# Kernel tuning notes

Measured on AMD Instinct MI355X. Metric: run time of the kernel, lower is better.

The kernel has to match this reference:

```python
import jax, jax.numpy as jnp
import numpy as np

MODEL_DIM = 4096
HEAD_DIM = 128
N_HEADS = 32
N_KV_HEADS = 8
B = 2
S = 2048
ROPE_BASE = 10000.0


def _rope(v, pos):
    """Interleaved-pair rotary embedding (Llama style). v: [b, s, h, d]."""
    d = v.shape[-1]
    half = d // 2
    inv_freq = 1.0 / (ROPE_BASE ** (jnp.arange(half, dtype=jnp.float32) * 2.0 / d))
    t = pos + jnp.arange(v.shape[1], dtype=jnp.float32)          # [s]
    ang = t[:, None] * inv_freq                                   # [s, half]
    cos = jnp.cos(ang)[None, :, None, :].astype(v.dtype)          # [1, s, 1, half]
    sin = jnp.sin(ang)[None, :, None, :].astype(v.dtype)
    x1 = v[..., 0::2]
    x2 = v[..., 1::2]
    o1 = x1 * cos - x2 * sin
    o2 = x1 * sin + x2 * cos
    return jnp.stack([o1, o2], axis=-1).reshape(v.shape)


def setup_inputs() -> dict:
    key = jax.random.key(0)
    kx, kq, kk, kv, ko = jax.random.split(key, 5)
    wscale = MODEL_DIM ** -0.5  # keep pre-softmax logits in a sane range
    x = jax.random.normal(kx, (B, S, MODEL_DIM), dtype=jnp.float32)
    wq = jax.random.normal(kq, (HEAD_DIM * N_HEADS, MODEL_DIM), dtype=jnp.float32) * wscale
    wk = jax.random.normal(kk, (HEAD_DIM * N_KV_HEADS, MODEL_DIM), dtype=jnp.float32) * wscale
    wv = jax.random.normal(kv, (HEAD_DIM * N_KV_HEADS, MODEL_DIM), dtype=jnp.float32) * wscale
    wo = jax.random.normal(ko, (HEAD_DIM * N_HEADS, MODEL_DIM), dtype=jnp.float32).T * wscale
    wo = jnp.asarray(wo)  # [MODEL_DIM, HEAD_DIM*N_HEADS] like nn.Linear weight
    # causal additive mask, as SDPA attn_mask (float): 0 on/below diag, -inf above
    causal = jnp.tril(jnp.ones((S, S), dtype=bool))
    mask = jnp.where(causal, 0.0, -jnp.inf).astype(jnp.float32)
    return {"x": x, "wq": wq, "wk": wk, "wv": wv, "wo": wo, "mask": mask, "pos": 0}


def reference(x, wq, wk, wv, wo, mask, pos):
    b, s, _ = x.shape
    rep = N_HEADS // N_KV_HEADS
    q = (x @ wq.T).reshape(b, s, N_HEADS, HEAD_DIM)
    k = (x @ wk.T).reshape(b, s, N_KV_HEADS, HEAD_DIM)
    v = (x @ wv.T).reshape(b, s, N_KV_HEADS, HEAD_DIM)
    q = _rope(q, pos)
    k = _rope(k, pos)
    # With pos=0 prefill, the kv-cache slice [:, :pos+s] equals k, v just written.
    # GQA without materializing repeat_interleave: group q heads by kv head.
    qg = q.reshape(b, s, N_KV_HEADS, rep, HEAD_DIM)
    scale = HEAD_DIM ** -0.5
    scores = jnp.einsum('bqhrd,bkhd->bhrqk', qg, k) * scale        # [b, kvh, rep, s, s]
    scores = scores + mask                                          # broadcast [s, s]
    p = jax.nn.softmax(scores, axis=-1)
    out = jnp.einsum('bhrqk,bkhd->bqhrd', p, v).reshape(b, s, N_HEADS * HEAD_DIM)
    return out @ wo.T
```

## Files before the change

kernel.cpp:

```cpp
#include <hip/hip_runtime.h>
#include <hip/hip_bf16.h>
#include <stdint.h>

#define MODEL_DIM 4096
#define HEAD_DIM  128
#define NH        32
#define NKV       8
#define BB        2
#define SS        2048
#define ROWS      (BB*SS)
#define QKVN      (MODEL_DIM + 2*NKV*HEAD_DIM)
#define KOFF      MODEL_DIM
#define VOFF      (MODEL_DIM + NKV*HEAD_DIM)
#define SCALE_QK  0.08838834764831845f

typedef __attribute__((ext_vector_type(8))) short short8;
typedef __attribute__((ext_vector_type(4))) float f32x4;

static __device__ __forceinline__ unsigned short f2bf(float f) {
  union { float f; unsigned u; } v; v.f = f;
  unsigned r = v.u + 0x7fffu + ((v.u >> 16) & 1u);
  return (unsigned short)(r >> 16);
}
static __device__ __forceinline__ float bf2f(unsigned short u) {
  union { unsigned u; float f; } v; v.u = ((unsigned)u) << 16;
  return v.f;
}
static __device__ __forceinline__ void glds16(const unsigned short* g, const unsigned short* l) {
  __builtin_amdgcn_global_load_lds((const __attribute__((address_space(1))) void*)g,
      (__attribute__((address_space(3))) void*)l, 16, 0, 0);
}

__global__ void cvt_bf16(const float* __restrict__ s, unsigned short* __restrict__ d, int n4) {
  int i = blockIdx.x * blockDim.x + threadIdx.x;
  int st = gridDim.x * blockDim.x;
  for (; i < n4; i += st) {
    float4 v = reinterpret_cast<const float4*>(s)[i];
    ushort4 o;
    o.x = f2bf(v.x); o.y = f2bf(v.y); o.z = f2bf(v.z); o.w = f2bf(v.w);
    reinterpret_cast<ushort4*>(d)[i] = o;
  }
}

template<int OUT_F32>
__global__ __launch_bounds__(256) void gemm_bt(
    const unsigned short* __restrict__ A, const unsigned short* __restrict__ B,
    void* __restrict__ Cv, int M, int N, int K)
{
  __shared__ unsigned short As[128 * 32];
  __shared__ unsigned short Bs[128 * 32];
  const int tid  = threadIdx.x;
  const int lane = tid & 63;
  const int w    = tid >> 6;

  const int nwg = gridDim.x;
  const int bid = blockIdx.x;
  const int q8  = nwg >> 3;
  const int wg  = (bid & 7) * q8 + (bid >> 3);
  const int gm  = M >> 7;
  const int bm  = wg % gm, bn = wg / gm;
  const int m0  = bm << 7, n0 = bn << 7;
  const int wm  = (w >> 1) << 6, wn = (w & 1) << 6;

  f32x4 acc[4][4] = {};

  const int rowA = lane >> 2;
  const int ch8  = (lane & 3) * 8;

  for (int k0 = 0; k0 < K; k0 += 32) {
    __syncthreads();
    #pragma unroll
    for (int i = 0; i < 2; ++i) {
      const unsigned short* ga = A + (size_t)(m0 + i*64 + w*16 + rowA) * K + k0 + ch8;
      glds16(ga, &As[(i*64 + w*16) * 32]);
      const unsigned short* gb = B + (size_t)(n0 + i*64 + w*16 + rowA) * K + k0 + ch8;
      glds16(gb, &Bs[(i*64 + w*16) * 32]);
    }
    __syncthreads();

    short8 af[4], bf[4];
    const int fr = lane & 15, fg = lane >> 4;
    #pragma unroll
    for (int r = 0; r < 4; ++r)
      af[r] = *(const short8*)&As[(wm + r*16 + fr) * 32 + fg * 8];
    #pragma unroll
    for (int r = 0; r < 4; ++r)
      bf[r] = *(const short8*)&Bs[(wn + r*16 + fr) * 32 + fg * 8];
    #pragma unroll
    for (int i = 0; i < 4; ++i)
      #pragma unroll
      for (int j = 0; j < 4; ++j)
        acc[i][j] = __builtin_amdgcn_mfma_f32_16x16x32_bf16(af[i], bf[j], acc[i][j], 0, 0, 0);
  }

  const int cr = (lane >> 4) * 4, cc = lane & 15;
  #pragma unroll
  for (int i = 0; i < 4; ++i)
    #pragma unroll
    for (int j = 0; j < 4; ++j) {
      const int gr = m0 + wm + i*16 + cr;
      const int gc = n0 + wn + j*16 + cc;
      #pragma unroll
      for (int e = 0; e < 4; ++e) {
        const float v = acc[i][j][e];
        if (OUT_F32) ((float*)Cv)[(size_t)(gr + e) * N + gc] = v;
        else ((unsigned short*)Cv)[(size_t)(gr + e) * N + gc] = f2bf(v);
      }
    }
}

__global__ void rope_kernel(unsigned short* __restrict__ qkv, const int* __restrict__ posp) {
  const int row = blockIdx.x;
  const float t = (float)((row & (SS - 1)) + posp[0]);
  const float c0 = -13.28771237954945f / 64.0f;
  for (int i = threadIdx.x; i < (NH + NKV) * 64; i += blockDim.x) {
    const int hh = i >> 6, p = i & 63;
    const int colbase = (hh < NH) ? hh * HEAD_DIM : KOFF + (hh - NH) * HEAD_DIM;
    const float inv = exp2f((float)p * c0);
    float sn, cs;
    sincosf(t * inv, &sn, &cs);
    const size_t base = (size_t)row * QKVN + colbase + 2 * p;
    const float x1 = bf2f(qkv[base]), x2 = bf2f(qkv[base + 1]);
    qkv[base]     = f2bf(x1 * cs - x2 * sn);
    qkv[base + 1] = f2bf(x1 * sn + x2 * cs);
  }
}

__global__ __launch_bounds__(256) void vtrans_kernel(
    const unsigned short* __restrict__ qkv, unsigned short* __restrict__ vt)
{
  __shared__ unsigned short T[64 * 128];
  const int tid = threadIdx.x;
  const int bk  = blockIdx.y;
  const int s0  = blockIdx.x * 64;
  const int b   = bk >> 3, kvh = bk & 7;

  #pragma unroll
  for (int it = 0; it < 4; ++it) {
    const int cid  = it * 256 + tid;
    const int s    = cid >> 4, slot = cid & 15;
    const int sl   = (slot & 8) | ((slot ^ (s >> 3)) & 7);
    *(uint4*)&T[s * 128 + sl * 8] =
      *(const uint4*)&qkv[(size_t)(b * SS + s0 + s) * QKVN + VOFF + kvh * HEAD_DIM + slot * 8];
  }
  __syncthreads();
  #pragma unroll
  for (int it = 0; it < 4; ++it) {
    const int cid = it * 256 + tid;
    const int d   = cid >> 3, s8 = (cid & 7) * 8;
    unsigned short tmp[8];
    #pragma unroll
    for (int j = 0; j < 8; ++j) {
      const int s    = s8 + j;
      const int slot = d >> 3;
      const int sl   = (slot & 8) | ((slot ^ (s >> 3)) & 7);
      tmp[j] = T[s * 128 + sl * 8 + (d & 7)];
    }
    *(uint4*)&vt[((size_t)bk * HEAD_DIM + d) * SS + s0 + s8] = *(uint4*)tmp;
  }
}

#define QBLK 64
#define KVB  64
#define LDP  72

static __device__ __forceinline__ float bcast_row16(float v0, float v1, float v2, float v3, int lane) {
  const int sel = (lane >> 2) & 3;
  const float a = (sel & 1) ? v1 : v0;
  const float b = (sel & 1) ? v3 : v2;
  const float m = (sel & 2) ? b : a;
  const int q = lane & 15;
  return __shfl(m, ((q >> 2) << 4) + ((q & 3) << 2));
}

__global__ __launch_bounds__(256) void attn_kernel(
    const unsigned short* __restrict__ qkv, const unsigned short* __restrict__ vt,
    unsigned short* __restrict__ out)
{
  __shared__ unsigned short Kb[2][KVB * HEAD_DIM];
  __shared__ unsigned short Vb[2][HEAD_DIM * KVB];
  __shared__ unsigned short Ps[4 * 16 * LDP];

  const int tid  = threadIdx.x;
  const int lane = tid & 63;
  const int w    = tid >> 6;
  const int bh   = blockIdx.y;
  const int b    = bh >> 5, h = bh & 31;
  const int kvh  = h >> 2;
  const int q0   = (gridDim.x - 1 - blockIdx.x) * QBLK;
  const int fr   = lane & 15, fg = lane >> 4;

  const unsigned short* kg  = qkv + KOFF + kvh * HEAD_DIM;
  const unsigned short* vtg = vt + (size_t)(b * NKV + kvh) * HEAD_DIM * SS;

  const size_t qrow0 = (size_t)(b * SS + q0 + w * 16);
  short8 qf[4];
  #pragma unroll
  for (int kk = 0; kk < 4; ++kk)
    qf[kk] = *(const short8*)&qkv[(qrow0 + fr) * QKVN + h * HEAD_DIM + kk * 32 + fg * 8];

  f32x4 ot[8] = {};
  float m_run[4], l_run[4];
  #pragma unroll
  for (int i = 0; i < 4; ++i) { m_run[i] = -INFINITY; l_run[i] = 0.f; }

  const int krow_l = lane >> 4;
  const int kslot  = lane & 15;
  const int vrow_l = lane >> 3;
  const int vslot  = lane & 7;

  const int ntile = (q0 >> 6) + 1;

  {
    const int j0 = 0;
    #pragma unroll
    for (int i = 0; i < 4; ++i) {
      const int r  = w * 16 + i * 4 + krow_l;
      const int gs = (kslot & 8) | ((kslot ^ r) & 7);
      glds16(kg + (size_t)(b * SS + j0 + r) * QKVN + gs * 8, &Kb[0][(w * 16 + i * 4) * 128]);
      const int d  = w * 32 + i * 8 + vrow_l;
      const int vg = vslot ^ (d & 7);
      glds16(vtg + (size_t)d * SS + j0 + vg * 8, &Vb[0][(w * 32 + i * 8) * 64]);
    }
  }

  int cur = 0;
  for (int jt = 0; jt < ntile; ++jt) {
    __syncthreads();
    if (jt + 1 < ntile) {
      const int j0n = (jt + 1) * KVB;
      #pragma unroll
      for (int i = 0; i < 4; ++i) {
        const int r  = w * 16 + i * 4 + krow_l;
        const int gs = (kslot & 8) | ((kslot ^ r) & 7);
        glds16(kg + (size_t)(b * SS + j0n + r) * QKVN + gs * 8, &Kb[cur ^ 1][(w * 16 + i * 4) * 128]);
        const int d  = w * 32 + i * 8 + vrow_l;
        const int vg = vslot ^ (d & 7);
        glds16(vtg + (size_t)d * SS + j0n + vg * 8, &Vb[cur ^ 1][(w * 32 + i * 8) * 64]);
      }
    }
    const unsigned short* Kc = Kb[cur];
    const unsigned short* Vc = Vb[cur];
    const bool diag = (jt == ntile - 1);

    float pv[4][4];
    #pragma unroll
    for (int ct = 0; ct < 4; ++ct) {
      f32x4 s = {};
      const int krow = ct * 16 + fr;
      #pragma unroll
      for (int kk = 0; kk < 4; ++kk) {
        const int c  = kk * 4 + fg;
        const int sl = (c & 8) | ((c ^ krow) & 7);
        const short8 kf = *(const short8*)&Kc[krow * 128 + sl * 8];
        s = __builtin_amdgcn_mfma_f32_16x16x32_bf16(qf[kk], kf, s, 0, 0, 0);
      }
      #pragma unroll
      for (int i = 0; i < 4; ++i) {
        float v = s[i] * SCALE_QK;
        if (diag) {
          const int qr = w * 16 + fg * 4 + i;
          const int kc = ct * 16 + fr;
          if (kc > qr) v = -INFINITY;
        }
        pv[ct][i] = v;
      }
    }

    float resc[4];
    #pragma unroll
    for (int i = 0; i < 4; ++i) {
      float mx = fmaxf(fmaxf(pv[0][i], pv[1][i]), fmaxf(pv[2][i], pv[3][i]));
      #pragma unroll
      for (int d = 1; d < 16; d <<= 1) mx = fmaxf(mx, __shfl_xor(mx, d));
      const float nm = fmaxf(m_run[i], mx);
      resc[i] = expf(m_run[i] - nm);
      m_run[i] = nm;
      float sum = 0.f;
      #pragma unroll
      for (int ct = 0; ct < 4; ++ct) {
        const float e = expf(pv[ct][i] - nm);
        pv[ct][i] = e;
        sum += e;
      }
      #pragma unroll
      for (int d = 1; d < 16; d <<= 1) sum += __shfl_xor(sum, d);
      l_run[i] = l_run[i] * resc[i] + sum;
    }

    unsigned short* Pw = &Ps[w * 16 * LDP];
    #pragma unroll
    for (int ct = 0; ct < 4; ++ct)
      #pragma unroll
      for (int i = 0; i < 4; ++i)
        Pw[(fg * 4 + i) * LDP + ct * 16 + fr] = f2bf(pv[ct][i]);

    const float rq = bcast_row16(resc[0], resc[1], resc[2], resc[3], lane);
    #pragma unroll
    for (int oc = 0; oc < 8; ++oc)
      #pragma unroll
      for (int e = 0; e < 4; ++e) ot[oc][e] *= rq;

    #pragma unroll
    for (int kk2 = 0; kk2 < 2; ++kk2) {
      const short8 pf = *(const short8*)&Pw[fr * LDP + kk2 * 32 + fg * 8];
      #pragma unroll
      for (int oc = 0; oc < 8; ++oc) {
        const int vd = oc * 16 + fr;
        const int sl = (kk2 * 4 + fg) ^ (vd & 7);
        const short8 vf = *(const short8*)&Vc[vd * 64 + sl * 8];
        ot[oc] = __builtin_amdgcn_mfma_f32_16x16x32_bf16(vf, pf, ot[oc], 0, 0, 0);
      }
    }
    cur ^= 1;
  }

  const float invq = bcast_row16(1.f / l_run[0], 1.f / l_run[1],
                                 1.f / l_run[2], 1.f / l_run[3], lane);
  const size_t orow = (size_t)(b * SS + q0 + w * 16) + (lane & 15);
  #pragma unroll
  for (int oc = 0; oc < 8; ++oc) {
    const unsigned short e0 = f2bf(ot[oc][0] * invq);
    const unsigned short e1 = f2bf(ot[oc][1] * invq);
    const unsigned short e2 = f2bf(ot[oc][2] * invq);
    const unsigned short e3 = f2bf(ot[oc][3] * invq);
    const uint2 val = make_uint2((unsigned)e0 | ((unsigned)e1 << 16),
                                 (unsigned)e2 | ((unsigned)e3 << 16));
    *(uint2*)&out[orow * MODEL_DIM + h * HEAD_DIM + oc * 16 + fg * 4] = val;
  }
}

extern "C" void kernel_launch(void* const* d_in, const int* in_sizes, int n_in,
                              void* d_out, int out_size, void* d_ws, size_t ws_size,
                              hipStream_t stream) {
  const float* x  = (const float*)d_in[0];
  const float* wq = (const float*)d_in[1];
  const float* wk = (const float*)d_in[2];
  const float* wv = (const float*)d_in[3];
  const float* wo = (const float*)d_in[4];
  const int* pos  = (const int*)d_in[6];
  float* out = (float*)d_out;

  unsigned short* xb   = (unsigned short*)d_ws;
  unsigned short* wqkv = xb   + (size_t)ROWS * MODEL_DIM;
  unsigned short* wob  = wqkv + (size_t)QKVN * MODEL_DIM;
  unsigned short* qkv  = wob  + (size_t)MODEL_DIM * MODEL_DIM;
  unsigned short* attn = qkv  + (size_t)ROWS * QKVN;
  unsigned short* vtb  = xb;

  cvt_bf16<<<2048, 256, 0, stream>>>(x,  xb,   ROWS * MODEL_DIM / 4);
  cvt_bf16<<<2048, 256, 0, stream>>>(wq, wqkv, MODEL_DIM * MODEL_DIM / 4);
  cvt_bf16<<<1024, 256, 0, stream>>>(wk, wqkv + (size_t)MODEL_DIM * MODEL_DIM,          NKV * HEAD_DIM * MODEL_DIM / 4);
  cvt_bf16<<<1024, 256, 0, stream>>>(wv, wqkv + (size_t)(MODEL_DIM + NKV * HEAD_DIM) * MODEL_DIM, NKV * HEAD_DIM * MODEL_DIM / 4);
  cvt_bf16<<<2048, 256, 0, stream>>>(wo, wob,  MODEL_DIM * MODEL_DIM / 4);

  gemm_bt<0><<<dim3((ROWS / 128) * (QKVN / 128)), 256, 0, stream>>>(xb, wqkv, qkv, ROWS, QKVN, MODEL_DIM);
  rope_kernel<<<ROWS, 256, 0, stream>>>(qkv, pos);
  vtrans_kernel<<<dim3(SS / 64, BB * NKV), 256, 0, stream>>>(qkv, vtb);
  attn_kernel<<<dim3(SS / QBLK, BB * NH), 256, 0, stream>>>(qkv, vtb, attn);
  gemm_bt<1><<<dim3((ROWS / 128) * (MODEL_DIM / 128)), 256, 0, stream>>>(attn, wob, out, ROWS, MODEL_DIM, MODEL_DIM);
}
```

Before: 1.106 ms.

## Transpose QK^T MFMA so P stays in registers, use exp2 softmax

Swaps the MFMA operands so each lane holds one query row's scores, so the P tile feeds the PV MFMA directly from registers. This removes the LDS round trip for P and the row-broadcast shuffles. The V transpose kernel permutes key order within 32-key groups to match the new register layout of P. Softmax now uses exp2 with a log2e-folded scale and a single per-lane running max and sum. The cost is tighter coupling between the V layout and the MFMA fragment mapping.

```diff
diff --git a/kernel.cpp b/kernel.cpp
--- a/kernel.cpp
+++ b/kernel.cpp
@@ -13,6 +13,7 @@
 #define KOFF      MODEL_DIM
 #define VOFF      (MODEL_DIM + NKV*HEAD_DIM)
 #define SCALE_QK  0.08838834764831845f
+#define SCALE_E2  0.12753102198681652f
 
 typedef __attribute__((ext_vector_type(8))) short short8;
 typedef __attribute__((ext_vector_type(4))) float f32x4;
@@ -151,10 +152,11 @@
     unsigned short tmp[8];
     #pragma unroll
     for (int j = 0; j < 8; ++j) {
-      const int s    = s8 + j;
+      const int so   = s8 + j;
+      const int si   = (so & 0x23) | ((so & 4) << 2) | ((so & 0x18) >> 1);
       const int slot = d >> 3;
-      const int sl   = (slot & 8) | ((slot ^ (s >> 3)) & 7);
-      tmp[j] = T[s * 128 + sl * 8 + (d & 7)];
+      const int sl   = (slot & 8) | ((slot ^ (si >> 3)) & 7);
+      tmp[j] = T[si * 128 + sl * 8 + (d & 7)];
     }
     *(uint4*)&vt[((size_t)bk * HEAD_DIM + d) * SS + s0 + s8] = *(uint4*)tmp;
   }
@@ -162,16 +164,6 @@
 
 #define QBLK 64
 #define KVB  64
-#define LDP  72
-
-static __device__ __forceinline__ float bcast_row16(float v0, float v1, float v2, float v3, int lane) {
-  const int sel = (lane >> 2) & 3;
-  const float a = (sel & 1) ? v1 : v0;
-  const float b = (sel & 1) ? v3 : v2;
-  const float m = (sel & 2) ? b : a;
-  const int q = lane & 15;
-  return __shfl(m, ((q >> 2) << 4) + ((q & 3) << 2));
-}
 
 __global__ __launch_bounds__(256) void attn_kernel(
     const unsigned short* __restrict__ qkv, const unsigned short* __restrict__ vt,
@@ -179,7 +171,6 @@
 {
   __shared__ unsigned short Kb[2][KVB * HEAD_DIM];
   __shared__ unsigned short Vb[2][HEAD_DIM * KVB];
-  __shared__ unsigned short Ps[4 * 16 * LDP];
 
   const int tid  = threadIdx.x;
   const int lane = tid & 63;
@@ -200,9 +191,7 @@
     qf[kk] = *(const short8*)&qkv[(qrow0 + fr) * QKVN + h * HEAD_DIM + kk * 32 + fg * 8];
 
   f32x4 ot[8] = {};
-  float m_run[4], l_run[4];
-  #pragma unroll
-  for (int i = 0; i < 4; ++i) { m_run[i] = -INFINITY; l_run[i] = 0.f; }
+  float m_run = -INFINITY, l_run = 0.f;
 
   const int krow_l = lane >> 4;
   const int kslot  = lane & 15;
@@ -212,15 +201,14 @@
   const int ntile = (q0 >> 6) + 1;
 
   {
-    const int j0 = 0;
     #pragma unroll
     for (int i = 0; i < 4; ++i) {
       const int r  = w * 16 + i * 4 + krow_l;
       const int gs = (kslot & 8) | ((kslot ^ r) & 7);
-      glds16(kg + (size_t)(b * SS + j0 + r) * QKVN + gs * 8, &Kb[0][(w * 16 + i * 4) * 128]);
+      glds16(kg + (size_t)(b * SS + r) * QKVN + gs * 8, &Kb[0][(w * 16 + i * 4) * 128]);
       const int d  = w * 32 + i * 8 + vrow_l;
       const int vg = vslot ^ (d & 7);
-      glds16(vtg + (size_t)d * SS + j0 + vg * 8, &Vb[0][(w * 32 + i * 8) * 64]);
+      glds16(vtg + (size_t)d * SS + vg * 8, &Vb[0][(w * 32 + i * 8) * 64]);
     }
   }
 
@@ -243,7 +231,7 @@
     const unsigned short* Vc = Vb[cur];
     const bool diag = (jt == ntile - 1);
 
-    float pv[4][4];
+    float p[4][4];
     #pragma unroll
     for (int ct = 0; ct < 4; ++ct) {
       f32x4 s = {};
@@ -253,57 +241,60 @@
         const int c  = kk * 4 + fg;
         const int sl = (c & 8) | ((c ^ krow) & 7);
         const short8 kf = *(const short8*)&Kc[krow * 128 + sl * 8];
-        s = __builtin_amdgcn_mfma_f32_16x16x32_bf16(qf[kk], kf, s, 0, 0, 0);
-      }
-      #pragma unroll
-      for (int i = 0; i < 4; ++i) {
-        float v = s[i] * SCALE_QK;
+        s = __builtin_amdgcn_mfma_f32_16x16x32_bf16(kf, qf[kk], s, 0, 0, 0);
+      }
+      #pragma unroll
+      for (int e = 0; e < 4; ++e) {
+        float v = s[e] * SCALE_E2;
         if (diag) {
-          const int qr = w * 16 + fg * 4 + i;
-          const int kc = ct * 16 + fr;
+          const int kc = ct * 16 + fg * 4 + e;
+          const int qr = w * 16 + fr;
           if (kc > qr) v = -INFINITY;
         }
-        pv[ct][i] = v;
-      }
-    }
-
-    float resc[4];
-    #pragma unroll
-    for (int i = 0; i < 4; ++i) {
-      float mx = fmaxf(fmaxf(pv[0][i], pv[1][i]), fmaxf(pv[2][i], pv[3][i]));
-      #pragma unroll
-      for (int d = 1; d < 16; d <<= 1) mx = fmaxf(mx, __shfl_xor(mx, d));
-      const float nm = fmaxf(m_run[i], mx);
-      resc[i] = expf(m_run[i] - nm);
-      m_run[i] = nm;
-      float sum = 0.f;
-      #pragma unroll
-      for (int ct = 0; ct < 4; ++ct) {
-        const float e = expf(pv[ct][i] - nm);
-        pv[ct][i] = e;
-        sum += e;
-      }
-      #pragma unroll
-      for (int d = 1; d < 16; d <<= 1) sum += __shfl_xor(sum, d);
-      l_run[i] = l_run[i] * resc[i] + sum;
-    }
-
-    unsigned short* Pw = &Ps[w * 16 * LDP];
+        p[ct][e] = v;
+      }
+    }
+
+    float mx = p[0][0];
     #pragma unroll
     for (int ct = 0; ct < 4; ++ct)
       #pragma unroll
-      for (int i = 0; i < 4; ++i)
-        Pw[(fg * 4 + i) * LDP + ct * 16 + fr] = f2bf(pv[ct][i]);
-
-    const float rq = bcast_row16(resc[0], resc[1], resc[2], resc[3], lane);
+      for (int e = 0; e < 4; ++e) mx = fmaxf(mx, p[ct][e]);
+    mx = fmaxf(mx, __shfl_xor(mx, 16));
+    mx = fmaxf(mx, __shfl_xor(mx, 32));
+    const float nm   = fmaxf(m_run, mx);
+    const float resc = exp2f(m_run - nm);
+    m_run = nm;
+    float sum = 0.f;
+    #pragma unroll
+    for (int ct = 0; ct < 4; ++ct)
+      #pragma unroll
+      for (int e = 0; e < 4; ++e) {
+        const float pe = exp2f(p[ct][e] - nm);
+        p[ct][e] = pe;
+        sum += pe;
+      }
+    sum += __shfl_xor(sum, 16);
+    sum += __shfl_xor(sum, 32);
+    l_run = l_run * resc + sum;
+
+    short8 pf0, pf1;
+    #pragma unroll
+    for (int e = 0; e < 4; ++e) {
+      pf0[e]     = (short)f2bf(p[0][e]);
+      pf0[e + 4] = (short)f2bf(p[1][e]);
+      pf1[e]     = (short)f2bf(p[2][e]);
+      pf1[e + 4] = (short)f2bf(p[3][e]);
+    }
+
     #pragma unroll
     for (int oc = 0; oc < 8; ++oc)
       #pragma unroll
-      for (int e = 0; e < 4; ++e) ot[oc][e] *= rq;
+      for (int e = 0; e < 4; ++e) ot[oc][e] *= resc;
 
     #pragma unroll
     for (int kk2 = 0; kk2 < 2; ++kk2) {
-      const short8 pf = *(const short8*)&Pw[fr * LDP + kk2 * 32 + fg * 8];
+      const short8 pf = kk2 ? pf1 : pf0;
       #pragma unroll
       for (int oc = 0; oc < 8; ++oc) {
         const int vd = oc * 16 + fr;
@@ -315,8 +306,7 @@
     cur ^= 1;
   }
 
-  const float invq = bcast_row16(1.f / l_run[0], 1.f / l_run[1],
-                                 1.f / l_run[2], 1.f / l_run[3], lane);
+  const float invq = 1.f / l_run;
   const size_t orow = (size_t)(b * SS + q0 + w * 16) + (lane & 15);
   #pragma unroll
   for (int oc = 0; oc < 8; ++oc) {
```

New measurement: 976.7 us. 1.13x faster.
